# Performance work log

Hardware: AMD Instinct MI355X
Metric: run time of the kernel (lower is better)

The kernel has to match this reference:

```python
import jax, jax.numpy as jnp
import numpy as np

N_NODES = 50000
N_EDGES = 1000000
D = 64          # input feature dim
H = 64          # hidden dim per conv layer / pooling out dim
N_GRAPHS = 256  # number of graphs in the batch


def setup_inputs() -> dict:
    key = jax.random.key(0)
    ks = jax.random.split(key, 10)
    x = jax.random.normal(ks[0], (N_NODES, D), dtype=jnp.float32)
    edge_index = jax.random.randint(ks[1], (2, N_EDGES), 0, N_NODES, dtype=jnp.int64)
    batch = jnp.sort(jax.random.randint(ks[2], (N_NODES,), 0, N_GRAPHS, dtype=jnp.int64))
    scale_in = 1.0 / np.sqrt(D)
    scale_h = 1.0 / np.sqrt(H)
    W1 = jax.random.normal(ks[3], (D, H), dtype=jnp.float32) * scale_in
    W2 = jax.random.normal(ks[4], (H, H), dtype=jnp.float32) * scale_h
    W3 = jax.random.normal(ks[5], (H, H), dtype=jnp.float32) * scale_h
    Wp1 = jax.random.normal(ks[6], (H, H), dtype=jnp.float32) * scale_h
    Wp2 = jax.random.normal(ks[7], (H, H), dtype=jnp.float32) * scale_h
    Wp3 = jax.random.normal(ks[8], (H, H), dtype=jnp.float32) * scale_h
    return {"x": x, "edge_index": edge_index, "batch": batch,
            "W1": W1, "W2": W2, "W3": W3,
            "Wp1": Wp1, "Wp2": Wp2, "Wp3": Wp3}


def _gcn_conv(x, W, src, dst):
    # PyG GCNConv with normalize=False, bias=False:
    #   h = x @ W; out[i] = sum_{(j->i) in E} h[j]   (no self-loops, unit edge weight)
    h = x @ W                                   # [N, H]
    return jax.ops.segment_sum(h[src], dst, num_segments=N_NODES)  # [N, H]


def reference(x, edge_index, batch, W1, W2, W3, Wp1, Wp2, Wp3):
    src, dst = edge_index[0], edge_index[1]
    x1 = jax.nn.relu(_gcn_conv(x, W1, src, dst))    # layer 0 output
    x2 = jax.nn.relu(_gcn_conv(x1, W2, src, dst))   # layer 1 output
    x3 = jax.nn.relu(_gcn_conv(x2, W3, src, dst))   # layer 2 output
    # Pooling: global_add_pool per layer output -> per-layer Linear -> stack -> sum -> relu
    p1 = jax.ops.segment_sum(x1, batch, num_segments=N_GRAPHS) @ Wp1  # [G, H]
    p2 = jax.ops.segment_sum(x2, batch, num_segments=N_GRAPHS) @ Wp2
    p3 = jax.ops.segment_sum(x3, batch, num_segments=N_GRAPHS) @ Wp3
    return jax.nn.relu(p1 + p2 + p3)                # [G, H]
```

## Files before the change

kernel.cpp:

```cpp
#include <hip/hip_runtime.h>
#include <hip/hip_bf16.h>

#define NN 50000
#define NE 1000000
#define DIM 64
#define NG 256
#define NBUCK 196
#define ROUND 4096
#define NBLK 245
#define TOT2D (NBUCK * NBLK)
#define SCANB 47

__global__ __launch_bounds__(512) void hist2d_kernel(const int* __restrict__ dst,
                                                     int* __restrict__ hist,
                                                     float* __restrict__ pool) {
    int gtid = blockIdx.x * 512 + threadIdx.x;
    for (int i = gtid; i < 3 * NG * DIM; i += NBLK * 512) pool[i] = 0.f;

    __shared__ int h[NBUCK];
    int t = threadIdx.x;
    if (t < NBUCK) h[t] = 0;
    __syncthreads();
    int base = blockIdx.x * ROUND;
#pragma unroll
    for (int it = 0; it < 8; ++it) {
        int e = base + it * 512 + t;
        if (e < NE) atomicAdd(&h[dst[e] >> 8], 1);
    }
    __syncthreads();
    if (t < NBUCK) hist[t * NBLK + blockIdx.x] = h[t];
}

__global__ __launch_bounds__(1024) void scanA_kernel(const int* __restrict__ hist,
                                                     int* __restrict__ blocksum) {
    __shared__ int tmp[1024];
    int t = threadIdx.x;
    int i = blockIdx.x * 1024 + t;
    tmp[t] = (i < TOT2D) ? hist[i] : 0;
    __syncthreads();
    for (int s = 512; s > 0; s >>= 1) {
        if (t < s) tmp[t] += tmp[t + s];
        __syncthreads();
    }
    if (t == 0) blocksum[blockIdx.x] = tmp[0];
}

__global__ __launch_bounds__(64) void scanB_kernel(int* __restrict__ blocksum) {
    __shared__ int tmp[64];
    int t = threadIdx.x;
    int v = (t < SCANB) ? blocksum[t] : 0;
    tmp[t] = v;
    __syncthreads();
    for (int off = 1; off < 64; off <<= 1) {
        int a = (t >= off) ? tmp[t - off] : 0;
        __syncthreads();
        tmp[t] += a;
        __syncthreads();
    }
    if (t < SCANB) blocksum[t] = tmp[t] - v;
}

__global__ __launch_bounds__(1024) void scanC_kernel(const int* __restrict__ hist,
                                                     const int* __restrict__ blocksum,
                                                     int* __restrict__ scanned) {
    __shared__ int tmp[1024];
    int t = threadIdx.x;
    int i = blockIdx.x * 1024 + t;
    int v = (i < TOT2D) ? hist[i] : 0;
    tmp[t] = v;
    __syncthreads();
    for (int off = 1; off < 1024; off <<= 1) {
        int a = (t >= off) ? tmp[t - off] : 0;
        __syncthreads();
        tmp[t] += a;
        __syncthreads();
    }
    if (i < TOT2D) scanned[i] = tmp[t] - v + blocksum[blockIdx.x];
}

__global__ __launch_bounds__(512) void permute_kernel(
    const int* __restrict__ src, const int* __restrict__ dst,
    const int* __restrict__ scanned, unsigned int* __restrict__ bucketed) {
    __shared__ int cur[NBUCK];
    int t = threadIdx.x;
    int blk = blockIdx.x;
    if (t < NBUCK) cur[t] = scanned[t * NBLK + blk];
    __syncthreads();
    int base = blk * ROUND;
#pragma unroll
    for (int it = 0; it < 8; ++it) {
        int e = base + it * 512 + t;
        if (e < NE) {
            int d = dst[e];
            int s = src[e];
            int b = d >> 8;
            int pos = atomicAdd(&cur[b], 1);
            bucketed[pos] = ((unsigned int)(d & 255) << 16) | (unsigned int)s;
        }
    }
}

__global__ __launch_bounds__(512) void bucket_sort_kernel(
    const unsigned int* __restrict__ bucketed, const int* __restrict__ scanned,
    int* __restrict__ offsets, int* __restrict__ csr) {
    __shared__ int hist[256];
    __shared__ int sc[256];
    __shared__ int cur[256];
    int b = blockIdx.x;
    int t = threadIdx.x;
    if (t < 256) hist[t] = 0;
    __syncthreads();
    int gbase = scanned[b * NBLK];
    int gend  = (b < NBUCK - 1) ? scanned[(b + 1) * NBLK] : NE;
    int count = gend - gbase;
    const unsigned int* bd = bucketed + gbase;
    for (int e = t; e < count; e += 512) atomicAdd(&hist[bd[e] >> 16], 1);
    __syncthreads();
    if (t < 256) sc[t] = hist[t];
    __syncthreads();
    for (int off = 1; off < 256; off <<= 1) {
        int a = 0;
        if (t < 256 && t >= off) a = sc[t - off];
        __syncthreads();
        if (t < 256) sc[t] += a;
        __syncthreads();
    }
    if (t < 256) {
        int excl = sc[t] - hist[t];
        cur[t] = excl;
        int node = b * 256 + t;
        if (node < NN) offsets[node] = gbase + excl;
    }
    if (b == NBUCK - 1 && t == 0) offsets[NN] = NE;
    __syncthreads();
    for (int e = t; e < count; e += 512) {
        unsigned int v = bd[e];
        int p = atomicAdd(&cur[v >> 16], 1);
        csr[gbase + p] = (int)(v & 0xFFFFu);
    }
}

__global__ __launch_bounds__(128) void gemm64_kernel(const float* __restrict__ X,
                                                     const float* __restrict__ W,
                                                     __hip_bfloat16* __restrict__ H,
                                                     int nrows) {
    __shared__ float Xl[128 * 65];
    int t = threadIdx.x;
    int base = blockIdx.x * 128;
    for (int idx = t; idx < 128 * 16; idx += 128) {
        int row = idx >> 4;
        int c4  = idx & 15;
        float4 v = make_float4(0.f, 0.f, 0.f, 0.f);
        if (base + row < nrows)
            v = *reinterpret_cast<const float4*>(&X[(size_t)(base + row) * 64 + c4 * 4]);
        float* p = &Xl[row * 65 + c4 * 4];
        p[0] = v.x; p[1] = v.y; p[2] = v.z; p[3] = v.w;
    }
    __syncthreads();
    float acc[64];
#pragma unroll
    for (int c = 0; c < 64; ++c) acc[c] = 0.f;
#pragma unroll 4
    for (int k = 0; k < 64; ++k) {
        float xv = Xl[t * 65 + k];
#pragma unroll
        for (int c4 = 0; c4 < 16; ++c4) {
            float4 w = *reinterpret_cast<const float4*>(&W[k * 64 + c4 * 4]);
            acc[c4 * 4 + 0] = fmaf(xv, w.x, acc[c4 * 4 + 0]);
            acc[c4 * 4 + 1] = fmaf(xv, w.y, acc[c4 * 4 + 1]);
            acc[c4 * 4 + 2] = fmaf(xv, w.z, acc[c4 * 4 + 2]);
            acc[c4 * 4 + 3] = fmaf(xv, w.w, acc[c4 * 4 + 3]);
        }
    }
    int row = base + t;
    if (row < nrows) {
        alignas(16) __hip_bfloat16 hb[64];
#pragma unroll
        for (int c = 0; c < 64; ++c) hb[c] = __float2bfloat16(acc[c]);
        uint4* dst4 = reinterpret_cast<uint4*>(&H[(size_t)row * 64]);
        const uint4* src4 = reinterpret_cast<const uint4*>(hb);
#pragma unroll
        for (int q = 0; q < 8; ++q) dst4[q] = src4[q];
    }
}

template <bool WRITE_X>
__global__ void gather_kernel(const __hip_bfloat16* __restrict__ H,
                              const int* __restrict__ offsets,
                              const int* __restrict__ csr, const int* __restrict__ batch,
                              float* __restrict__ Xout, float* __restrict__ pool) {
    int tid = blockIdx.x * blockDim.x + threadIdx.x;
    int lane = tid & 63;
    int gw = tid >> 6;
    int nw = (gridDim.x * blockDim.x) >> 6;
    int chunk = (NN + nw - 1) / nw;
    int start = gw * chunk;
    if (start >= NN) return;
    int stop = min(start + chunk, NN);
    float pacc = 0.f;
    int curg = batch[start];
    for (int n = start; n < stop; ++n) {
        int beg = offsets[n], end = offsets[n + 1];
        float a0 = 0.f, a1 = 0.f, a2 = 0.f, a3 = 0.f;
        float a4 = 0.f, a5 = 0.f, a6 = 0.f, a7 = 0.f;
        int i = beg;
        for (; i + 8 <= end; i += 8) {
            int s0 = csr[i],     s1 = csr[i + 1], s2 = csr[i + 2], s3 = csr[i + 3];
            int s4 = csr[i + 4], s5 = csr[i + 5], s6 = csr[i + 6], s7 = csr[i + 7];
            a0 += __bfloat162float(H[(size_t)s0 * 64 + lane]);
            a1 += __bfloat162float(H[(size_t)s1 * 64 + lane]);
            a2 += __bfloat162float(H[(size_t)s2 * 64 + lane]);
            a3 += __bfloat162float(H[(size_t)s3 * 64 + lane]);
            a4 += __bfloat162float(H[(size_t)s4 * 64 + lane]);
            a5 += __bfloat162float(H[(size_t)s5 * 64 + lane]);
            a6 += __bfloat162float(H[(size_t)s6 * 64 + lane]);
            a7 += __bfloat162float(H[(size_t)s7 * 64 + lane]);
        }
        if (i + 4 <= end) {
            int s0 = csr[i], s1 = csr[i + 1], s2 = csr[i + 2], s3 = csr[i + 3];
            a0 += __bfloat162float(H[(size_t)s0 * 64 + lane]);
            a1 += __bfloat162float(H[(size_t)s1 * 64 + lane]);
            a2 += __bfloat162float(H[(size_t)s2 * 64 + lane]);
            a3 += __bfloat162float(H[(size_t)s3 * 64 + lane]);
            i += 4;
        }
        for (; i < end; ++i) a0 += __bfloat162float(H[(size_t)csr[i] * 64 + lane]);
        float v = fmaxf(((a0 + a1) + (a2 + a3)) + ((a4 + a5) + (a6 + a7)), 0.f);
        if (WRITE_X) Xout[(size_t)n * 64 + lane] = v;
        int g = batch[n];
        if (g != curg) {
            unsafeAtomicAdd(&pool[(size_t)curg * 64 + lane], pacc);
            pacc = 0.f; curg = g;
        }
        pacc += v;
    }
    unsafeAtomicAdd(&pool[(size_t)curg * 64 + lane], pacc);
}

__global__ void final_kernel(const float* __restrict__ P1, const float* __restrict__ P2,
                             const float* __restrict__ P3,
                             const float* __restrict__ Wp1, const float* __restrict__ Wp2,
                             const float* __restrict__ Wp3, float* __restrict__ out) {
    int g = blockIdx.x;
    int c = threadIdx.x;
    float acc = 0.f;
#pragma unroll
    for (int k = 0; k < 64; ++k) {
        acc = fmaf(P1[g * 64 + k], Wp1[k * 64 + c], acc);
        acc = fmaf(P2[g * 64 + k], Wp2[k * 64 + c], acc);
        acc = fmaf(P3[g * 64 + k], Wp3[k * 64 + c], acc);
    }
    out[g * 64 + c] = fmaxf(acc, 0.f);
}

extern "C" void kernel_launch(void* const* d_in, const int* in_sizes, int n_in,
                              void* d_out, int out_size, void* d_ws, size_t ws_size,
                              hipStream_t stream) {
    const float* x     = (const float*)d_in[0];
    const int*   eidx  = (const int*)d_in[1];
    const int*   batch = (const int*)d_in[2];
    const float* W1  = (const float*)d_in[3];
    const float* W2  = (const float*)d_in[4];
    const float* W3  = (const float*)d_in[5];
    const float* Wp1 = (const float*)d_in[6];
    const float* Wp2 = (const float*)d_in[7];
    const float* Wp3 = (const float*)d_in[8];
    float* out = (float*)d_out;

    const int* src = eidx;
    const int* dst = eidx + NE;

    __hip_bfloat16* bufH = (__hip_bfloat16*)d_ws;
    float* bufX  = (float*)(bufH + (size_t)NN * DIM);
    float* pool1 = bufX + (size_t)NN * DIM;
    float* pool2 = pool1 + (size_t)NG * DIM;
    float* pool3 = pool2 + (size_t)NG * DIM;
    int* hist     = (int*)(pool3 + (size_t)NG * DIM);
    int* scanned  = hist + TOT2D;
    int* blocksum = scanned + TOT2D;
    int* offsets  = blocksum + 64;
    unsigned int* bucketed = (unsigned int*)(offsets + NN + 1);
    int* csr      = (int*)(bucketed + NE);

    hist2d_kernel<<<NBLK, 512, 0, stream>>>(dst, hist, pool1);
    scanA_kernel<<<SCANB, 1024, 0, stream>>>(hist, blocksum);
    scanB_kernel<<<1, 64, 0, stream>>>(blocksum);
    scanC_kernel<<<SCANB, 1024, 0, stream>>>(hist, blocksum, scanned);
    permute_kernel<<<NBLK, 512, 0, stream>>>(src, dst, scanned, bucketed);
    bucket_sort_kernel<<<NBUCK, 512, 0, stream>>>(bucketed, scanned, offsets, csr);

    const int gemm_blocks = (NN + 127) / 128;
    const int gath_blocks = 1792;

    gemm64_kernel<<<gemm_blocks, 128, 0, stream>>>(x, W1, bufH, NN);
    gather_kernel<true><<<gath_blocks, 256, 0, stream>>>(bufH, offsets, csr, batch, bufX, pool1);
    gemm64_kernel<<<gemm_blocks, 128, 0, stream>>>(bufX, W2, bufH, NN);
    gather_kernel<true><<<gath_blocks, 256, 0, stream>>>(bufH, offsets, csr, batch, bufX, pool2);
    gemm64_kernel<<<gemm_blocks, 128, 0, stream>>>(bufX, W3, bufH, NN);
    gather_kernel<false><<<gath_blocks, 256, 0, stream>>>(bufH, offsets, csr, batch, nullptr, pool3);

    final_kernel<<<NG, 64, 0, stream>>>(pool1, pool2, pool3, Wp1, Wp2, Wp3, out);
}
```

Measured before the change: 295.4 us.

## Gather 8 edges per wavefront with 16-byte bf16 row loads and shuffle reduce

Restructures the neighbor-gather so each wavefront splits into 8 edge groups of 8 lanes. Each lane loads 16 bytes (8 bf16 channels) of a source row, and partial sums are combined with xor shuffles. Previously each lane loaded one 2-byte bf16 element per edge. The goal is fewer, wider memory instructions and more edges in flight per wavefront. The cost is shuffle-reduction overhead per node, partially idle lanes on low-degree nodes, and output/atomic writes done by only one lane group.

```diff
diff --git a/kernel.cpp b/kernel.cpp
--- a/kernel.cpp
+++ b/kernel.cpp
@@ -184,6 +184,10 @@
     }
 }
 
+#define ACC2(u, alo, ahi)                                           \
+    alo += __uint_as_float((u) << 16);                              \
+    ahi += __uint_as_float((u) & 0xffff0000u);
+
 template <bool WRITE_X>
 __global__ void gather_kernel(const __hip_bfloat16* __restrict__ H,
                               const int* __restrict__ offsets,
@@ -191,50 +195,72 @@
                               float* __restrict__ Xout, float* __restrict__ pool) {
     int tid = blockIdx.x * blockDim.x + threadIdx.x;
     int lane = tid & 63;
+    int egrp = lane >> 3;
+    int cpart = lane & 7;
     int gw = tid >> 6;
     int nw = (gridDim.x * blockDim.x) >> 6;
     int chunk = (NN + nw - 1) / nw;
     int start = gw * chunk;
     if (start >= NN) return;
     int stop = min(start + chunk, NN);
-    float pacc = 0.f;
+    float p0 = 0.f, p1 = 0.f, p2 = 0.f, p3 = 0.f, p4 = 0.f, p5 = 0.f, p6 = 0.f, p7 = 0.f;
     int curg = batch[start];
     for (int n = start; n < stop; ++n) {
         int beg = offsets[n], end = offsets[n + 1];
         float a0 = 0.f, a1 = 0.f, a2 = 0.f, a3 = 0.f;
         float a4 = 0.f, a5 = 0.f, a6 = 0.f, a7 = 0.f;
-        int i = beg;
-        for (; i + 8 <= end; i += 8) {
-            int s0 = csr[i],     s1 = csr[i + 1], s2 = csr[i + 2], s3 = csr[i + 3];
-            int s4 = csr[i + 4], s5 = csr[i + 5], s6 = csr[i + 6], s7 = csr[i + 7];
-            a0 += __bfloat162float(H[(size_t)s0 * 64 + lane]);
-            a1 += __bfloat162float(H[(size_t)s1 * 64 + lane]);
-            a2 += __bfloat162float(H[(size_t)s2 * 64 + lane]);
-            a3 += __bfloat162float(H[(size_t)s3 * 64 + lane]);
-            a4 += __bfloat162float(H[(size_t)s4 * 64 + lane]);
-            a5 += __bfloat162float(H[(size_t)s5 * 64 + lane]);
-            a6 += __bfloat162float(H[(size_t)s6 * 64 + lane]);
-            a7 += __bfloat162float(H[(size_t)s7 * 64 + lane]);
-        }
-        if (i + 4 <= end) {
-            int s0 = csr[i], s1 = csr[i + 1], s2 = csr[i + 2], s3 = csr[i + 3];
-            a0 += __bfloat162float(H[(size_t)s0 * 64 + lane]);
-            a1 += __bfloat162float(H[(size_t)s1 * 64 + lane]);
-            a2 += __bfloat162float(H[(size_t)s2 * 64 + lane]);
-            a3 += __bfloat162float(H[(size_t)s3 * 64 + lane]);
-            i += 4;
-        }
-        for (; i < end; ++i) a0 += __bfloat162float(H[(size_t)csr[i] * 64 + lane]);
-        float v = fmaxf(((a0 + a1) + (a2 + a3)) + ((a4 + a5) + (a6 + a7)), 0.f);
-        if (WRITE_X) Xout[(size_t)n * 64 + lane] = v;
+        for (int e0 = beg; e0 < end; e0 += 32) {
+            uint4 h0 = make_uint4(0, 0, 0, 0), h1 = h0, h2 = h0, h3 = h0;
+            int e;
+            e = e0 + egrp;
+            if (e < end) h0 = *reinterpret_cast<const uint4*>(&H[(size_t)csr[e] * 64 + cpart * 8]);
+            e = e0 + 8 + egrp;
+            if (e < end) h1 = *reinterpret_cast<const uint4*>(&H[(size_t)csr[e] * 64 + cpart * 8]);
+            e = e0 + 16 + egrp;
+            if (e < end) h2 = *reinterpret_cast<const uint4*>(&H[(size_t)csr[e] * 64 + cpart * 8]);
+            e = e0 + 24 + egrp;
+            if (e < end) h3 = *reinterpret_cast<const uint4*>(&H[(size_t)csr[e] * 64 + cpart * 8]);
+            ACC2(h0.x, a0, a1) ACC2(h0.y, a2, a3) ACC2(h0.z, a4, a5) ACC2(h0.w, a6, a7)
+            ACC2(h1.x, a0, a1) ACC2(h1.y, a2, a3) ACC2(h1.z, a4, a5) ACC2(h1.w, a6, a7)
+            ACC2(h2.x, a0, a1) ACC2(h2.y, a2, a3) ACC2(h2.z, a4, a5) ACC2(h2.w, a6, a7)
+            ACC2(h3.x, a0, a1) ACC2(h3.y, a2, a3) ACC2(h3.z, a4, a5) ACC2(h3.w, a6, a7)
+        }
+#pragma unroll
+        for (int m = 8; m <= 32; m <<= 1) {
+            a0 += __shfl_xor(a0, m, 64); a1 += __shfl_xor(a1, m, 64);
+            a2 += __shfl_xor(a2, m, 64); a3 += __shfl_xor(a3, m, 64);
+            a4 += __shfl_xor(a4, m, 64); a5 += __shfl_xor(a5, m, 64);
+            a6 += __shfl_xor(a6, m, 64); a7 += __shfl_xor(a7, m, 64);
+        }
+        float v0 = fmaxf(a0, 0.f), v1 = fmaxf(a1, 0.f), v2 = fmaxf(a2, 0.f), v3 = fmaxf(a3, 0.f);
+        float v4 = fmaxf(a4, 0.f), v5 = fmaxf(a5, 0.f), v6 = fmaxf(a6, 0.f), v7 = fmaxf(a7, 0.f);
+        if (WRITE_X && egrp == 0) {
+            float4* o = reinterpret_cast<float4*>(&Xout[(size_t)n * 64 + cpart * 8]);
+            o[0] = make_float4(v0, v1, v2, v3);
+            o[1] = make_float4(v4, v5, v6, v7);
+        }
         int g = batch[n];
         if (g != curg) {
-            unsafeAtomicAdd(&pool[(size_t)curg * 64 + lane], pacc);
-            pacc = 0.f; curg = g;
-        }
-        pacc += v;
-    }
-    unsafeAtomicAdd(&pool[(size_t)curg * 64 + lane], pacc);
+            if (egrp == 0) {
+                float* pp = &pool[(size_t)curg * 64 + cpart * 8];
+                unsafeAtomicAdd(pp + 0, p0); unsafeAtomicAdd(pp + 1, p1);
+                unsafeAtomicAdd(pp + 2, p2); unsafeAtomicAdd(pp + 3, p3);
+                unsafeAtomicAdd(pp + 4, p4); unsafeAtomicAdd(pp + 5, p5);
+                unsafeAtomicAdd(pp + 6, p6); unsafeAtomicAdd(pp + 7, p7);
+            }
+            p0 = p1 = p2 = p3 = p4 = p5 = p6 = p7 = 0.f;
+            curg = g;
+        }
+        p0 += v0; p1 += v1; p2 += v2; p3 += v3;
+        p4 += v4; p5 += v5; p6 += v6; p7 += v7;
+    }
+    if (egrp == 0) {
+        float* pp = &pool[(size_t)curg * 64 + cpart * 8];
+        unsafeAtomicAdd(pp + 0, p0); unsafeAtomicAdd(pp + 1, p1);
+        unsafeAtomicAdd(pp + 2, p2); unsafeAtomicAdd(pp + 3, p3);
+        unsafeAtomicAdd(pp + 4, p4); unsafeAtomicAdd(pp + 5, p5);
+        unsafeAtomicAdd(pp + 6, p6); unsafeAtomicAdd(pp + 7, p7);
+    }
 }
 
 __global__ void final_kernel(const float* __restrict__ P1, const float* __restrict__ P2,
```

Result: slower. 309.2 us (+4.7%).
